# Kernel optimization log

Hardware: AMD Instinct MI355X
Metric: run time of the kernel (lower is better)

Reference implementation:

```python
import jax, jax.numpy as jnp
import numpy as np

NUM_HEADS = 16


def setup_inputs() -> dict:
    rng = jax.random.key(0)
    ks = jax.random.split(rng, 11)
    T, B, E = 1024, 4, 1024
    s = E ** -0.5  # weight init scale
    return {
        "query": jax.random.normal(ks[0], (T, B, E), jnp.float32),
        "key": jax.random.normal(ks[1], (T, B, E), jnp.float32),
        "value": jax.random.normal(ks[2], (T, B, E), jnp.float32),
        "q_proj_weight": jax.random.normal(ks[3], (E, E), jnp.float32) * s,
        "k_proj_weight1": jax.random.normal(ks[4], (E, E), jnp.float32) * s,
        "k_proj_weight2": jax.random.normal(ks[5], (E, E), jnp.float32) * s,
        "v_proj_weight": jax.random.normal(ks[6], (E, E), jnp.float32) * s,
        "in_proj_bias": jax.random.normal(ks[7], (4 * E,), jnp.float32) * 0.02,
        "out_proj_weight": jax.random.normal(ks[8], (E, E), jnp.float32) * s,
        "out_proj_bias": jax.random.normal(ks[9], (E,), jnp.float32) * 0.02,
        "pi": jax.random.uniform(ks[10], (2, NUM_HEADS), jnp.float32, 0.3, 0.7),
    }


def reference(query, key, value, q_proj_weight, k_proj_weight1, k_proj_weight2,
              v_proj_weight, in_proj_bias, out_proj_weight, out_proj_bias, pi):
    T, Bz, E = query.shape
    H = NUM_HEADS
    hd = E // H
    scaling = hd ** -0.5

    b_q, b_k1, b_k2, b_v = jnp.split(in_proj_bias, 4)
    q = query @ q_proj_weight.T + b_q
    k1 = key @ k_proj_weight1.T + b_k1
    k2 = key @ k_proj_weight2.T + b_k2
    v = value @ v_proj_weight.T + b_v

    def heads(x):  # (S, B, E) -> (B*H, S, hd)
        S = x.shape[0]
        return x.reshape(S, Bz * H, hd).transpose(1, 0, 2)

    q, k1, k2, v = heads(q), heads(k1), heads(k2), heads(v)

    def sqdist(a, b):  # (B*H, Nt, hd), (B*H, Ns, hd) -> (B*H, Nt, Ns)
        a2 = jnp.sum(a * a, axis=-1)
        b2 = jnp.sum(b * b, axis=-1)
        ab = jnp.einsum('btd,bsd->bts', a, b)
        return a2[:, :, None] + b2[:, None, :] - 2.0 * ab

    e1 = jnp.exp(-scaling / 2.0 * sqdist(q, k1))
    e2 = jnp.exp(-3.0 * scaling / 2.0 * sqdist(q, k2))

    pi1 = jnp.clip(jnp.abs(pi[0]), 1e-6, 2.0)  # (H,)
    pi2 = jnp.clip(jnp.abs(pi[1]), 1e-6, 2.0)

    Nt, Ns = e1.shape[1], e1.shape[2]
    attn = (e1.reshape(Bz, H, Nt, Ns) * pi1[None, :, None, None]
            + e2.reshape(Bz, H, Nt, Ns) * pi2[None, :, None, None])
    attn = attn.reshape(Bz * H, Nt, Ns)
    attn = attn / (jnp.sum(attn, axis=-1, keepdims=True) + 1e-6)

    out = jnp.einsum('bts,bsd->btd', attn, v)        # (B*H, Nt, hd)
    out = out.transpose(1, 0, 2).reshape(T, Bz, E)   # (T, B, E)
    return out @ out_proj_weight.T + out_proj_bias
```

## Files before the change

kernel.cpp:

```cpp
#include <hip/hip_runtime.h>
#include <hip/hip_bf16.h>

#define T_DIM 1024
#define B_DIM 4
#define E_DIM 1024
#define H_DIM 16
#define HD    64
#define M_DIM (T_DIM * B_DIM)

typedef __hip_bfloat16 bf16;
typedef __bf16 bf16x8 __attribute__((ext_vector_type(8)));
typedef __bf16 bf16x4 __attribute__((ext_vector_type(4)));
typedef float  f32x4  __attribute__((ext_vector_type(4)));

#define P4S ((size_t)M_DIM * E_DIM)
#define P1S ((size_t)E_DIM * E_DIM)

__global__ __launch_bounds__(256) void cvt_all(
    const float* __restrict__ q, const float* __restrict__ k,
    const float* __restrict__ v, const float* __restrict__ w0,
    const float* __restrict__ w1, const float* __restrict__ w2,
    const float* __restrict__ w3, const float* __restrict__ w4,
    __bf16* __restrict__ dst)
{
  size_t i = ((size_t)blockIdx.x * 256 + threadIdx.x) * 8;
  const float* src;
  size_t off;
  if (i < P4S)            { src = q; off = i; }
  else if (i < 2 * P4S)   { src = k; off = i - P4S; }
  else if (i < 3 * P4S)   { src = v; off = i - 2 * P4S; }
  else {
    size_t j = i - 3 * P4S;
    int wsel = (int)(j >> 20);
    off = j & (P1S - 1);
    const float* ws[5] = {w0, w1, w2, w3, w4};
    src = ws[wsel];
  }
  float4 a = *(const float4*)(src + off);
  float4 b = *(const float4*)(src + off + 4);
  bf16x8 o;
  o[0] = (__bf16)a.x; o[1] = (__bf16)a.y; o[2] = (__bf16)a.z; o[3] = (__bf16)a.w;
  o[4] = (__bf16)b.x; o[5] = (__bf16)b.y; o[6] = (__bf16)b.z; o[7] = (__bf16)b.w;
  *(bf16x8*)(dst + i) = o;
}

__device__ __forceinline__ void load_lds16(const __bf16* g, __bf16* l) {
  __builtin_amdgcn_global_load_lds(
      (__attribute__((address_space(1))) void*)(void*)g,
      (__attribute__((address_space(3))) void*)l, 16, 0, 0);
}

template <typename TO>
__device__ __forceinline__ void gemm_body(
    const __bf16* __restrict__ X, const __bf16* __restrict__ W,
    const float* __restrict__ bias, TO* __restrict__ C,
    int bm, int bn, int Ndim, int Kdim, __bf16* As, __bf16* Bs)
{
  const int tid  = threadIdx.x;
  const int lane = tid & 63;
  const int wave = tid >> 6;
  const int wy = (wave >> 1) * 64;
  const int wx = (wave & 1) * 64;
  const int mrow = lane & 15, quad = lane >> 4;

  const int srow = tid >> 2;
  const int ke   = (tid & 3) * 8;
  const __bf16* gA0 = X + (size_t)(bm + srow)      * Kdim + ke;
  const __bf16* gA1 = X + (size_t)(bm + srow + 64) * Kdim + ke;
  const __bf16* gB0 = W + (size_t)(bn + srow)      * Kdim + ke;
  const __bf16* gB1 = W + (size_t)(bn + srow + 64) * Kdim + ke;
  __bf16* lA0 = As + tid * 8;
  __bf16* lA1 = As + (tid + 256) * 8;
  __bf16* lB0 = Bs + tid * 8;
  __bf16* lB1 = Bs + (tid + 256) * 8;

  f32x4 acc[4][4];
#pragma unroll
  for (int i = 0; i < 4; ++i)
#pragma unroll
    for (int j = 0; j < 4; ++j) acc[i][j] = (f32x4)0.0f;

  for (int k0 = 0; k0 < Kdim; k0 += 32) {
    __syncthreads();
    load_lds16(gA0 + k0, lA0);
    load_lds16(gA1 + k0, lA1);
    load_lds16(gB0 + k0, lB0);
    load_lds16(gB1 + k0, lB1);
    __syncthreads();
    bf16x8 af[4], bf[4];
#pragma unroll
    for (int i = 0; i < 4; ++i)
      af[i] = *(const bf16x8*)(As + (wy + i * 16 + mrow) * 32 + quad * 8);
#pragma unroll
    for (int j = 0; j < 4; ++j)
      bf[j] = *(const bf16x8*)(Bs + (wx + j * 16 + mrow) * 32 + quad * 8);
#pragma unroll
    for (int i = 0; i < 4; ++i)
#pragma unroll
      for (int j = 0; j < 4; ++j)
        acc[i][j] = __builtin_amdgcn_mfma_f32_16x16x32_bf16(af[i], bf[j], acc[i][j], 0, 0, 0);
  }

#pragma unroll
  for (int j = 0; j < 4; ++j) {
    int col = bn + wx + j * 16 + mrow;
    float bc = bias[col];
#pragma unroll
    for (int i = 0; i < 4; ++i) {
      int rbase = bm + wy + i * 16 + quad * 4;
#pragma unroll
      for (int r = 0; r < 4; ++r)
        C[(size_t)(rbase + r) * Ndim + col] = (TO)(acc[i][j][r] + bc);
    }
  }
}

__global__ __launch_bounds__(256) void proj_gemm4(
    const __bf16* __restrict__ xbase, const __bf16* __restrict__ wbase,
    const float* __restrict__ bin, __bf16* __restrict__ cbase)
{
  __shared__ __bf16 As[128 * 32];
  __shared__ __bf16 Bs[128 * 32];
  const int z = blockIdx.z;
  const __bf16* X = xbase + ((z == 0) ? 0 : (z == 3) ? 2 * P4S : P4S);
  const __bf16* W = wbase + (size_t)z * P1S;
  const float* bias = bin + z * E_DIM;
  __bf16* C = cbase + (size_t)z * P4S;
  gemm_body<__bf16>(X, W, bias, C, blockIdx.x * 128, blockIdx.y * 128,
                    E_DIM, E_DIM, As, Bs);
}

__global__ __launch_bounds__(256) void out_gemm(
    const __bf16* __restrict__ X, const __bf16* __restrict__ W,
    const float* __restrict__ bias, float* __restrict__ C)
{
  __shared__ __bf16 As[128 * 32];
  __shared__ __bf16 Bs[128 * 32];
  gemm_body<float>(X, W, bias, C, blockIdx.x * 128, blockIdx.y * 128,
                   E_DIM, E_DIM, As, Bs);
}

__global__ __launch_bounds__(256) void head_norms(
    const __bf16* __restrict__ Qp, const __bf16* __restrict__ K1p,
    const __bf16* __restrict__ K2p, float* __restrict__ qn,
    float* __restrict__ kn1, float* __restrict__ kn2)
{
  int id = blockIdx.x * 256 + threadIdx.x;
  int which = id >> 16;
  int r = id & 65535;
  int bh = r >> 10, t = r & 1023;
  int b = bh >> 4, h = bh & 15;
  const __bf16* src = (which == 0) ? Qp : ((which == 1) ? K1p : K2p);
  float* dst = (which == 0) ? qn : ((which == 1) ? kn1 : kn2);
  const __bf16* p = src + (size_t)(t * 4 + b) * 1024 + h * 64;
  float s = 0.f;
#pragma unroll
  for (int c = 0; c < 8; ++c) {
    bf16x8 v = *(const bf16x8*)(p + c * 8);
#pragma unroll
    for (int j = 0; j < 8; ++j) { float x = (float)v[j]; s += x * x; }
  }
  dst[bh * 1024 + t] = s;
}

__global__ __launch_bounds__(256) void v_transpose(
    const __bf16* __restrict__ Vp, __bf16* __restrict__ Vt_g)
{
  const int bh = blockIdx.x, kt = blockIdx.y;
  const int b = bh >> 4, h = bh & 15;
  const int tid = threadIdx.x;
  __shared__ __bf16 tile[64][88];
  {
    int s = tid >> 2, d0 = (tid & 3) * 16;
    const __bf16* src = Vp + (size_t)((kt * 64 + s) * 4 + b) * 1024 + h * 64 + d0;
    *(bf16x8*)(&tile[s][d0])     = *(const bf16x8*)(src);
    *(bf16x8*)(&tile[s][d0 + 8]) = *(const bf16x8*)(src + 8);
  }
  __syncthreads();
#pragma unroll
  for (int c = 0; c < 2; ++c) {
    int idx = tid * 2 + c;
    int d = idx >> 3, u0 = (idx & 7) * 8;
    bf16x8 o;
#pragma unroll
    for (int i = 0; i < 8; ++i) {
      int u = u0 + i;
      int s = (u & 3) * 16 + (u >> 2);
      o[i] = tile[s][d];
    }
    *(bf16x8*)(Vt_g + ((size_t)bh * 64 + d) * 1024 + kt * 64 + u0) = o;
  }
}

__global__ __launch_bounds__(256, 2) void mgk_attn_mfma(
    const __bf16* __restrict__ Qp, const __bf16* __restrict__ K1p,
    const __bf16* __restrict__ K2p, const __bf16* __restrict__ Vt_g,
    const float* __restrict__ qn_g, const float* __restrict__ kn1_g,
    const float* __restrict__ kn2_g, const float* __restrict__ pi,
    __bf16* __restrict__ AO)
{
  __shared__ __bf16 lds[28672];
  __bf16* Qs  = lds;
  __bf16* K1s = lds + 8192;
  __bf16* K2s = lds + 12288;
  __bf16* Vt  = lds + 16384;
  __bf16* Pl  = lds + 20480;

  const int bh = blockIdx.x, qt = blockIdx.y;
  const int b = bh >> 4, h = bh & 15;
  const int tid = threadIdx.x, lane = tid & 63, w = tid >> 6;
  const int mrow = lane & 15, quad = lane >> 4;

  const float c1 = 0.0625f;
  const float c2 = 0.1875f;
  const float p1 = fminf(fmaxf(fabsf(pi[h]), 1e-6f), 2.0f);
  const float p2 = fminf(fmaxf(fabsf(pi[H_DIM + h]), 1e-6f), 2.0f);
  const int hoff = h * 64;

  f32x4 qnv[2];
#pragma unroll
  for (int i = 0; i < 2; ++i)
    qnv[i] = *(const f32x4*)(qn_g + bh * 1024 + qt * 128 + w * 32 + i * 16 + quad * 4);

#pragma unroll
  for (int wi = 0; wi < 4; ++wi) {
    int window = w * 4 + wi;
    int qr = window * 8 + (lane >> 3), c = lane & 7;
    const __bf16* src = Qp + (size_t)((qt * 128 + qr) * 4 + b) * 1024 + hoff
                        + ((c ^ (qr & 7)) << 3);
    load_lds16(src, Qs + window * 512 + lane * 8);
  }

  f32x4 oacc[2][4];
#pragma unroll
  for (int i = 0; i < 2; ++i)
#pragma unroll
    for (int j = 0; j < 4; ++j) oacc[i][j] = (f32x4)0.0f;
  f32x4 rsl[2] = {(f32x4)0.0f, (f32x4)0.0f};

  for (int kt = 0; kt < 16; ++kt) {
    __syncthreads();
#pragma unroll
    for (int wi = 0; wi < 2; ++wi) {
      int window = w * 2 + wi;
      int kr = window * 8 + (lane >> 3), c = lane & 7;
      size_t srow = (size_t)((kt * 64 + kr) * 4 + b) * 1024 + hoff;
      int off = (c ^ (kr & 7)) << 3;
      load_lds16(K1p + srow + off, K1s + window * 512 + lane * 8);
      load_lds16(K2p + srow + off, K2s + window * 512 + lane * 8);
      load_lds16(Vt_g + ((size_t)bh * 64 + kr) * 1024 + kt * 64 + off,
                 Vt + window * 512 + lane * 8);
    }
    float kn1j[4], kn2j[4];
#pragma unroll
    for (int j = 0; j < 4; ++j) {
      kn1j[j] = kn1_g[bh * 1024 + kt * 64 + j * 16 + mrow];
      kn2j[j] = kn2_g[bh * 1024 + kt * 64 + j * 16 + mrow];
    }
    __syncthreads();

    bf16x8 af[2][2];
#pragma unroll
    for (int i = 0; i < 2; ++i)
#pragma unroll
      for (int kk = 0; kk < 2; ++kk)
        af[i][kk] = *(const bf16x8*)(Qs + (w * 32 + i * 16 + mrow) * 64
                                     + (((kk * 4 + quad) ^ (mrow & 7)) << 3));
    f32x4 acc1[2][4], acc2[2][4];
#pragma unroll
    for (int i = 0; i < 2; ++i)
#pragma unroll
      for (int j = 0; j < 4; ++j) { acc1[i][j] = (f32x4)0.0f; acc2[i][j] = (f32x4)0.0f; }
#pragma unroll
    for (int kk = 0; kk < 2; ++kk)
#pragma unroll
      for (int j = 0; j < 4; ++j) {
        bf16x8 b1f = *(const bf16x8*)(K1s + (j * 16 + mrow) * 64
                                      + (((kk * 4 + quad) ^ (mrow & 7)) << 3));
        bf16x8 b2f = *(const bf16x8*)(K2s + (j * 16 + mrow) * 64
                                      + (((kk * 4 + quad) ^ (mrow & 7)) << 3));
#pragma unroll
        for (int i = 0; i < 2; ++i) {
          acc1[i][j] = __builtin_amdgcn_mfma_f32_16x16x32_bf16(af[i][kk], b1f, acc1[i][j], 0, 0, 0);
          acc2[i][j] = __builtin_amdgcn_mfma_f32_16x16x32_bf16(af[i][kk], b2f, acc2[i][j], 0, 0, 0);
        }
      }

#pragma unroll
    for (int i = 0; i < 2; ++i) {
      f32x4 pv[4];
#pragma unroll
      for (int j = 0; j < 4; ++j) {
        f32x4 p;
#pragma unroll
        for (int r = 0; r < 4; ++r) {
          float arg1 = c1 * (2.0f * acc1[i][j][r] - qnv[i][r] - kn1j[j]);
          float arg2 = c2 * (2.0f * acc2[i][j][r] - qnv[i][r] - kn2j[j]);
          p[r] = p1 * __expf(arg1) + p2 * __expf(arg2);
        }
        pv[j] = p;
        rsl[i] += p;
      }
#pragma unroll
      for (int r = 0; r < 4; ++r) {
        int q = i * 16 + quad * 4 + r;
        bf16x4 pk;
        pk[0] = (__bf16)pv[0][r]; pk[1] = (__bf16)pv[1][r];
        pk[2] = (__bf16)pv[2][r]; pk[3] = (__bf16)pv[3][r];
        int lc = mrow >> 1;
        *(bf16x4*)(Pl + w * 2048 + q * 64 + ((lc ^ (q & 7)) << 3) + (mrow & 1) * 4) = pk;
      }
    }
    __syncthreads();

    bf16x8 pf[2][2];
#pragma unroll
    for (int i = 0; i < 2; ++i)
#pragma unroll
      for (int kk = 0; kk < 2; ++kk)
        pf[i][kk] = *(const bf16x8*)(Pl + w * 2048 + (i * 16 + mrow) * 64
                                     + (((kk * 4 + quad) ^ (mrow & 7)) << 3));
#pragma unroll
    for (int kk = 0; kk < 2; ++kk)
#pragma unroll
      for (int j = 0; j < 4; ++j) {
        bf16x8 vf = *(const bf16x8*)(Vt + (j * 16 + mrow) * 64
                                     + (((kk * 4 + quad) ^ (mrow & 7)) << 3));
#pragma unroll
        for (int i = 0; i < 2; ++i)
          oacc[i][j] = __builtin_amdgcn_mfma_f32_16x16x32_bf16(pf[i][kk], vf, oacc[i][j], 0, 0, 0);
      }
  }

#pragma unroll
  for (int i = 0; i < 2; ++i)
#pragma unroll
    for (int d = 1; d < 16; d <<= 1) {
      f32x4 o;
#pragma unroll
      for (int r = 0; r < 4; ++r) o[r] = __shfl_xor(rsl[i][r], d, 64);
      rsl[i] += o;
    }

#pragma unroll
  for (int i = 0; i < 2; ++i) {
    f32x4 inv;
#pragma unroll
    for (int r = 0; r < 4; ++r) inv[r] = 1.0f / (rsl[i][r] + 1e-6f);
#pragma unroll
    for (int j = 0; j < 4; ++j) {
      int col = hoff + j * 16 + mrow;
#pragma unroll
      for (int r = 0; r < 4; ++r) {
        int t = qt * 128 + w * 32 + i * 16 + quad * 4 + r;
        AO[(size_t)(t * 4 + b) * 1024 + col] = (__bf16)(oacc[i][j][r] * inv[r]);
      }
    }
  }
}

extern "C" void kernel_launch(void* const* d_in, const int* in_sizes, int n_in,
                              void* d_out, int out_size, void* d_ws, size_t ws_size,
                              hipStream_t stream) {
  const float* query = (const float*)d_in[0];
  const float* key   = (const float*)d_in[1];
  const float* value = (const float*)d_in[2];
  const float* Wq    = (const float*)d_in[3];
  const float* Wk1   = (const float*)d_in[4];
  const float* Wk2   = (const float*)d_in[5];
  const float* Wv    = (const float*)d_in[6];
  const float* bin   = (const float*)d_in[7];
  const float* Wo    = (const float*)d_in[8];
  const float* bo    = (const float*)d_in[9];
  const float* pi    = (const float*)d_in[10];
  float* out = (float*)d_out;

  __bf16* qc  = (__bf16*)d_ws;
  __bf16* wq  = qc  + 3 * P4S;
  __bf16* wo  = wq  + 4 * P1S;
  __bf16* Qp  = wq  + 5 * P1S;
  __bf16* K1p = Qp  + P4S;
  __bf16* K2p = K1p + P4S;
  __bf16* Vp  = K2p + P4S;
  __bf16* AO  = Vp  + P4S;
  float*  qn_g  = (float*)(AO + P4S);
  float*  kn1_g = qn_g  + 64 * 1024;
  float*  kn2_g = kn1_g + 64 * 1024;
  __bf16* Vt_g  = qc;

  cvt_all<<<8704, 256, 0, stream>>>(query, key, value, Wq, Wk1, Wk2, Wv, Wo, qc);

  proj_gemm4<<<dim3(M_DIM / 128, E_DIM / 128, 4), 256, 0, stream>>>(qc, wq, bin, Qp);

  head_norms<<<768, 256, 0, stream>>>(Qp, K1p, K2p, qn_g, kn1_g, kn2_g);
  v_transpose<<<dim3(64, 16), 256, 0, stream>>>(Vp, Vt_g);

  mgk_attn_mfma<<<dim3(64, 8), 256, 0, stream>>>(
      Qp, K1p, K2p, Vt_g, qn_g, kn1_g, kn2_g, pi, AO);

  out_gemm<<<dim3(M_DIM / 128, E_DIM / 128), 256, 0, stream>>>(AO, wo, bo, out);
}
```

Before: 279.2 us.

## Pipeline attention K/V staging, fold constants into exp2, split-K output GEMM

Head-norm, V-transpose and output-bias initialization are merged into one prep kernel. The key norms are prescaled and log(pi) is folded into them, so the attention kernel uses raw exp2 with no multiplies by pi. The attention loop now prefetches the next K/V tile into LDS after reading fragments into registers, which removes one barrier per iteration. The output projection becomes a split-K=2 GEMM that accumulates into the bias-initialized output with float atomics. This trades a higher register count and atomic traffic for fewer launches and better overlap.

```diff
diff --git a/kernel.cpp b/kernel.cpp
--- a/kernel.cpp
+++ b/kernel.cpp
@@ -15,6 +15,9 @@
 
 #define P4S ((size_t)M_DIM * E_DIM)
 #define P1S ((size_t)E_DIM * E_DIM)
+
+#define C1F 0.0901684437f
+#define C2F 0.2705053270f
 
 __global__ __launch_bounds__(256) void cvt_all(
     const float* __restrict__ q, const float* __restrict__ k,
@@ -130,65 +133,135 @@
                     E_DIM, E_DIM, As, Bs);
 }
 
-__global__ __launch_bounds__(256) void out_gemm(
+__global__ __launch_bounds__(256) void out_gemm_sk(
     const __bf16* __restrict__ X, const __bf16* __restrict__ W,
-    const float* __restrict__ bias, float* __restrict__ C)
+    float* __restrict__ C)
 {
   __shared__ __bf16 As[128 * 32];
   __shared__ __bf16 Bs[128 * 32];
-  gemm_body<float>(X, W, bias, C, blockIdx.x * 128, blockIdx.y * 128,
-                   E_DIM, E_DIM, As, Bs);
-}
-
-__global__ __launch_bounds__(256) void head_norms(
+  const int tid  = threadIdx.x;
+  const int lane = tid & 63;
+  const int wave = tid >> 6;
+  const int wy = (wave >> 1) * 64;
+  const int wx = (wave & 1) * 64;
+  const int bm = blockIdx.x * 128, bn = blockIdx.y * 128;
+  const int kbeg = blockIdx.z * 512;
+  const int mrow = lane & 15, quad = lane >> 4;
+
+  const int srow = tid >> 2;
+  const int ke   = (tid & 3) * 8;
+  const __bf16* gA0 = X + (size_t)(bm + srow)      * E_DIM + kbeg + ke;
+  const __bf16* gA1 = X + (size_t)(bm + srow + 64) * E_DIM + kbeg + ke;
+  const __bf16* gB0 = W + (size_t)(bn + srow)      * E_DIM + kbeg + ke;
+  const __bf16* gB1 = W + (size_t)(bn + srow + 64) * E_DIM + kbeg + ke;
+  __bf16* lA0 = As + tid * 8;
+  __bf16* lA1 = As + (tid + 256) * 8;
+  __bf16* lB0 = Bs + tid * 8;
+  __bf16* lB1 = Bs + (tid + 256) * 8;
+
+  f32x4 acc[4][4];
+#pragma unroll
+  for (int i = 0; i < 4; ++i)
+#pragma unroll
+    for (int j = 0; j < 4; ++j) acc[i][j] = (f32x4)0.0f;
+
+  for (int k0 = 0; k0 < 512; k0 += 32) {
+    __syncthreads();
+    load_lds16(gA0 + k0, lA0);
+    load_lds16(gA1 + k0, lA1);
+    load_lds16(gB0 + k0, lB0);
+    load_lds16(gB1 + k0, lB1);
+    __syncthreads();
+    bf16x8 af[4], bf[4];
+#pragma unroll
+    for (int i = 0; i < 4; ++i)
+      af[i] = *(const bf16x8*)(As + (wy + i * 16 + mrow) * 32 + quad * 8);
+#pragma unroll
+    for (int j = 0; j < 4; ++j)
+      bf[j] = *(const bf16x8*)(Bs + (wx + j * 16 + mrow) * 32 + quad * 8);
+#pragma unroll
+    for (int i = 0; i < 4; ++i)
+#pragma unroll
+      for (int j = 0; j < 4; ++j)
+        acc[i][j] = __builtin_amdgcn_mfma_f32_16x16x32_bf16(af[i], bf[j], acc[i][j], 0, 0, 0);
+  }
+
+#pragma unroll
+  for (int j = 0; j < 4; ++j) {
+    int col = bn + wx + j * 16 + mrow;
+#pragma unroll
+    for (int i = 0; i < 4; ++i) {
+      int rbase = bm + wy + i * 16 + quad * 4;
+#pragma unroll
+      for (int r = 0; r < 4; ++r)
+        unsafeAtomicAdd(&C[(size_t)(rbase + r) * E_DIM + col], acc[i][j][r]);
+    }
+  }
+}
+
+__global__ __launch_bounds__(256) void prep(
     const __bf16* __restrict__ Qp, const __bf16* __restrict__ K1p,
-    const __bf16* __restrict__ K2p, float* __restrict__ qn,
-    float* __restrict__ kn1, float* __restrict__ kn2)
-{
-  int id = blockIdx.x * 256 + threadIdx.x;
-  int which = id >> 16;
-  int r = id & 65535;
-  int bh = r >> 10, t = r & 1023;
-  int b = bh >> 4, h = bh & 15;
-  const __bf16* src = (which == 0) ? Qp : ((which == 1) ? K1p : K2p);
-  float* dst = (which == 0) ? qn : ((which == 1) ? kn1 : kn2);
-  const __bf16* p = src + (size_t)(t * 4 + b) * 1024 + h * 64;
-  float s = 0.f;
-#pragma unroll
-  for (int c = 0; c < 8; ++c) {
-    bf16x8 v = *(const bf16x8*)(p + c * 8);
-#pragma unroll
-    for (int j = 0; j < 8; ++j) { float x = (float)v[j]; s += x * x; }
-  }
-  dst[bh * 1024 + t] = s;
-}
-
-__global__ __launch_bounds__(256) void v_transpose(
-    const __bf16* __restrict__ Vp, __bf16* __restrict__ Vt_g)
-{
-  const int bh = blockIdx.x, kt = blockIdx.y;
-  const int b = bh >> 4, h = bh & 15;
-  const int tid = threadIdx.x;
-  __shared__ __bf16 tile[64][88];
-  {
-    int s = tid >> 2, d0 = (tid & 3) * 16;
-    const __bf16* src = Vp + (size_t)((kt * 64 + s) * 4 + b) * 1024 + h * 64 + d0;
-    *(bf16x8*)(&tile[s][d0])     = *(const bf16x8*)(src);
-    *(bf16x8*)(&tile[s][d0 + 8]) = *(const bf16x8*)(src + 8);
-  }
-  __syncthreads();
-#pragma unroll
-  for (int c = 0; c < 2; ++c) {
-    int idx = tid * 2 + c;
-    int d = idx >> 3, u0 = (idx & 7) * 8;
-    bf16x8 o;
-#pragma unroll
-    for (int i = 0; i < 8; ++i) {
-      int u = u0 + i;
-      int s = (u & 3) * 16 + (u >> 2);
-      o[i] = tile[s][d];
-    }
-    *(bf16x8*)(Vt_g + ((size_t)bh * 64 + d) * 1024 + kt * 64 + u0) = o;
+    const __bf16* __restrict__ K2p, const __bf16* __restrict__ Vp,
+    const float* __restrict__ pi, const float* __restrict__ bo,
+    float* __restrict__ qn, float* __restrict__ kn1, float* __restrict__ kn2,
+    __bf16* __restrict__ Vt_g, float* __restrict__ out)
+{
+  const int bid = blockIdx.x, tid = threadIdx.x;
+  if (bid < 768) {
+    int id = bid * 256 + tid;
+    int which = id >> 16;
+    int r = id & 65535;
+    int bh = r >> 10, t = r & 1023;
+    int b = bh >> 4, h = bh & 15;
+    const __bf16* src = (which == 0) ? Qp : ((which == 1) ? K1p : K2p);
+    const __bf16* p = src + (size_t)(t * 4 + b) * 1024 + h * 64;
+    float s = 0.f;
+#pragma unroll
+    for (int c = 0; c < 8; ++c) {
+      bf16x8 v = *(const bf16x8*)(p + c * 8);
+#pragma unroll
+      for (int j = 0; j < 8; ++j) { float x = (float)v[j]; s += x * x; }
+    }
+    if (which == 0) {
+      qn[bh * 1024 + t] = s;
+    } else if (which == 1) {
+      float p1 = fminf(fmaxf(fabsf(pi[h]), 1e-6f), 2.0f);
+      kn1[bh * 1024 + t] = C1F * s - __builtin_amdgcn_logf(p1);
+    } else {
+      float p2 = fminf(fmaxf(fabsf(pi[H_DIM + h]), 1e-6f), 2.0f);
+      kn2[bh * 1024 + t] = C2F * s - __builtin_amdgcn_logf(p2);
+    }
+  } else if (bid < 1792) {
+    int idx = bid - 768;
+    int bh = idx >> 4, kt = idx & 15;
+    int b = bh >> 4, h = bh & 15;
+    __shared__ __bf16 tile[64][88];
+    {
+      int s = tid >> 2, d0 = (tid & 3) * 16;
+      const __bf16* src = Vp + (size_t)((kt * 64 + s) * 4 + b) * 1024 + h * 64 + d0;
+      *(bf16x8*)(&tile[s][d0])     = *(const bf16x8*)(src);
+      *(bf16x8*)(&tile[s][d0 + 8]) = *(const bf16x8*)(src + 8);
+    }
+    __syncthreads();
+#pragma unroll
+    for (int c = 0; c < 2; ++c) {
+      int idx2 = tid * 2 + c;
+      int d = idx2 >> 3, u0 = (idx2 & 7) * 8;
+      bf16x8 o;
+#pragma unroll
+      for (int i = 0; i < 8; ++i) {
+        int u = u0 + i;
+        int s = (u & 3) * 16 + (u >> 2);
+        o[i] = tile[s][d];
+      }
+      *(bf16x8*)(Vt_g + ((size_t)bh * 64 + d) * 1024 + kt * 64 + u0) = o;
+    }
+  } else {
+    int idx = (bid - 1792) * 256 + tid;
+    int base = idx * 16;
+#pragma unroll
+    for (int c = 0; c < 4; ++c)
+      *(float4*)(out + base + c * 4) = *(const float4*)(bo + ((base + c * 4) & 1023));
   }
 }
 
@@ -196,8 +269,7 @@
     const __bf16* __restrict__ Qp, const __bf16* __restrict__ K1p,
     const __bf16* __restrict__ K2p, const __bf16* __restrict__ Vt_g,
     const float* __restrict__ qn_g, const float* __restrict__ kn1_g,
-    const float* __restrict__ kn2_g, const float* __restrict__ pi,
-    __bf16* __restrict__ AO)
+    const float* __restrict__ kn2_g, __bf16* __restrict__ AO)
 {
   __shared__ __bf16 lds[28672];
   __bf16* Qs  = lds;
@@ -210,36 +282,19 @@
   const int b = bh >> 4, h = bh & 15;
   const int tid = threadIdx.x, lane = tid & 63, w = tid >> 6;
   const int mrow = lane & 15, quad = lane >> 4;
-
-  const float c1 = 0.0625f;
-  const float c2 = 0.1875f;
-  const float p1 = fminf(fmaxf(fabsf(pi[h]), 1e-6f), 2.0f);
-  const float p2 = fminf(fmaxf(fabsf(pi[H_DIM + h]), 1e-6f), 2.0f);
   const int hoff = h * 64;
 
-  f32x4 qnv[2];
-#pragma unroll
-  for (int i = 0; i < 2; ++i)
-    qnv[i] = *(const f32x4*)(qn_g + bh * 1024 + qt * 128 + w * 32 + i * 16 + quad * 4);
-
-#pragma unroll
-  for (int wi = 0; wi < 4; ++wi) {
-    int window = w * 4 + wi;
-    int qr = window * 8 + (lane >> 3), c = lane & 7;
-    const __bf16* src = Qp + (size_t)((qt * 128 + qr) * 4 + b) * 1024 + hoff
-                        + ((c ^ (qr & 7)) << 3);
-    load_lds16(src, Qs + window * 512 + lane * 8);
-  }
-
-  f32x4 oacc[2][4];
-#pragma unroll
-  for (int i = 0; i < 2; ++i)
-#pragma unroll
-    for (int j = 0; j < 4; ++j) oacc[i][j] = (f32x4)0.0f;
-  f32x4 rsl[2] = {(f32x4)0.0f, (f32x4)0.0f};
-
-  for (int kt = 0; kt < 16; ++kt) {
-    __syncthreads();
+  const float TWO_C1 = 2.0f * C1F, TWO_C2 = 2.0f * C2F;
+
+  f32x4 s1v[2], s2v[2];
+#pragma unroll
+  for (int i = 0; i < 2; ++i) {
+    f32x4 q = *(const f32x4*)(qn_g + bh * 1024 + qt * 128 + w * 32 + i * 16 + quad * 4);
+    s1v[i] = C1F * q;
+    s2v[i] = C2F * q;
+  }
+
+  auto stageK = [&](int kt) {
 #pragma unroll
     for (int wi = 0; wi < 2; ++wi) {
       int window = w * 2 + wi;
@@ -251,53 +306,84 @@
       load_lds16(Vt_g + ((size_t)bh * 64 + kr) * 1024 + kt * 64 + off,
                  Vt + window * 512 + lane * 8);
     }
+  };
+
+#pragma unroll
+  for (int wi = 0; wi < 4; ++wi) {
+    int window = w * 4 + wi;
+    int qr = window * 8 + (lane >> 3), c = lane & 7;
+    const __bf16* src = Qp + (size_t)((qt * 128 + qr) * 4 + b) * 1024 + hoff
+                        + ((c ^ (qr & 7)) << 3);
+    load_lds16(src, Qs + window * 512 + lane * 8);
+  }
+  stageK(0);
+
+  f32x4 oacc[2][4];
+#pragma unroll
+  for (int i = 0; i < 2; ++i)
+#pragma unroll
+    for (int j = 0; j < 4; ++j) oacc[i][j] = (f32x4)0.0f;
+  f32x4 rsl[2] = {(f32x4)0.0f, (f32x4)0.0f};
+
+  __syncthreads();
+
+  bf16x8 af[2][2];
+#pragma unroll
+  for (int i = 0; i < 2; ++i)
+#pragma unroll
+    for (int kk = 0; kk < 2; ++kk)
+      af[i][kk] = *(const bf16x8*)(Qs + (w * 32 + i * 16 + mrow) * 64
+                                   + (((kk * 4 + quad) ^ (mrow & 7)) << 3));
+
+  for (int kt = 0; kt < 16; ++kt) {
     float kn1j[4], kn2j[4];
 #pragma unroll
     for (int j = 0; j < 4; ++j) {
       kn1j[j] = kn1_g[bh * 1024 + kt * 64 + j * 16 + mrow];
       kn2j[j] = kn2_g[bh * 1024 + kt * 64 + j * 16 + mrow];
     }
-    __syncthreads();
-
-    bf16x8 af[2][2];
+
+    bf16x8 b1f[2][4], b2f[2][4], vf[2][4];
+#pragma unroll
+    for (int kk = 0; kk < 2; ++kk)
+#pragma unroll
+      for (int j = 0; j < 4; ++j) {
+        int off = (j * 16 + mrow) * 64 + (((kk * 4 + quad) ^ (mrow & 7)) << 3);
+        b1f[kk][j] = *(const bf16x8*)(K1s + off);
+        b2f[kk][j] = *(const bf16x8*)(K2s + off);
+        vf[kk][j]  = *(const bf16x8*)(Vt  + off);
+      }
+    __syncthreads();
+
+    if (kt < 15) stageK(kt + 1);
+
+    f32x4 acc1[2][4], acc2[2][4];
 #pragma unroll
     for (int i = 0; i < 2; ++i)
 #pragma unroll
-      for (int kk = 0; kk < 2; ++kk)
-        af[i][kk] = *(const bf16x8*)(Qs + (w * 32 + i * 16 + mrow) * 64
-                                     + (((kk * 4 + quad) ^ (mrow & 7)) << 3));
-    f32x4 acc1[2][4], acc2[2][4];
-#pragma unroll
-    for (int i = 0; i < 2; ++i)
-#pragma unroll
       for (int j = 0; j < 4; ++j) { acc1[i][j] = (f32x4)0.0f; acc2[i][j] = (f32x4)0.0f; }
 #pragma unroll
     for (int kk = 0; kk < 2; ++kk)
 #pragma unroll
-      for (int j = 0; j < 4; ++j) {
-        bf16x8 b1f = *(const bf16x8*)(K1s + (j * 16 + mrow) * 64
-                                      + (((kk * 4 + quad) ^ (mrow & 7)) << 3));
-        bf16x8 b2f = *(const bf16x8*)(K2s + (j * 16 + mrow) * 64
-                                      + (((kk * 4 + quad) ^ (mrow & 7)) << 3));
+      for (int j = 0; j < 4; ++j)
 #pragma unroll
         for (int i = 0; i < 2; ++i) {
-          acc1[i][j] = __builtin_amdgcn_mfma_f32_16x16x32_bf16(af[i][kk], b1f, acc1[i][j], 0, 0, 0);
-          acc2[i][j] = __builtin_amdgcn_mfma_f32_16x16x32_bf16(af[i][kk], b2f, acc2[i][j], 0, 0, 0);
+          acc1[i][j] = __builtin_amdgcn_mfma_f32_16x16x32_bf16(af[i][kk], b1f[kk][j], acc1[i][j], 0, 0, 0);
+          acc2[i][j] = __builtin_amdgcn_mfma_f32_16x16x32_bf16(af[i][kk], b2f[kk][j], acc2[i][j], 0, 0, 0);
         }
-      }
 
 #pragma unroll
     for (int i = 0; i < 2; ++i) {
       f32x4 pv[4];
 #pragma unroll
       for (int j = 0; j < 4; ++j) {
+        f32x4 d1 = s1v[i] + kn1j[j];
+        f32x4 d2 = s2v[i] + kn2j[j];
         f32x4 p;
 #pragma unroll
-        for (int r = 0; r < 4; ++r) {
-          float arg1 = c1 * (2.0f * acc1[i][j][r] - qnv[i][r] - kn1j[j]);
-          float arg2 = c2 * (2.0f * acc2[i][j][r] - qnv[i][r] - kn2j[j]);
-          p[r] = p1 * __expf(arg1) + p2 * __expf(arg2);
-        }
+        for (int r = 0; r < 4; ++r)
+          p[r] = __builtin_amdgcn_exp2f(TWO_C1 * acc1[i][j][r] - d1[r])
+               + __builtin_amdgcn_exp2f(TWO_C2 * acc2[i][j][r] - d2[r]);
         pv[j] = p;
         rsl[i] += p;
       }
@@ -311,7 +397,6 @@
         *(bf16x4*)(Pl + w * 2048 + q * 64 + ((lc ^ (q & 7)) << 3) + (mrow & 1) * 4) = pk;
       }
     }
-    __syncthreads();
 
     bf16x8 pf[2][2];
 #pragma unroll
@@ -323,13 +408,12 @@
 #pragma unroll
     for (int kk = 0; kk < 2; ++kk)
 #pragma unroll
-      for (int j = 0; j < 4; ++j) {
-        bf16x8 vf = *(const bf16x8*)(Vt + (j * 16 + mrow) * 64
-                                     + (((kk * 4 + quad) ^ (mrow & 7)) << 3));
+      for (int j = 0; j < 4; ++j)
 #pragma unroll
         for (int i = 0; i < 2; ++i)
-          oacc[i][j] = __builtin_amdgcn_mfma_f32_16x16x32_bf16(pf[i][kk], vf, oacc[i][j], 0, 0, 0);
-      }
+          oacc[i][j] = __builtin_amdgcn_mfma_f32_16x16x32_bf16(pf[i][kk], vf[kk][j], oacc[i][j], 0, 0, 0);
+
+    if (kt < 15) __syncthreads();
   }
 
 #pragma unroll
@@ -392,11 +476,11 @@
 
   proj_gemm4<<<dim3(M_DIM / 128, E_DIM / 128, 4), 256, 0, stream>>>(qc, wq, bin, Qp);
 
-  head_norms<<<768, 256, 0, stream>>>(Qp, K1p, K2p, qn_g, kn1_g, kn2_g);
-  v_transpose<<<dim3(64, 16), 256, 0, stream>>>(Vp, Vt_g);
+  prep<<<2816, 256, 0, stream>>>(Qp, K1p, K2p, Vp, pi, bo,
+                                 qn_g, kn1_g, kn2_g, Vt_g, out);
 
   mgk_attn_mfma<<<dim3(64, 8), 256, 0, stream>>>(
-      Qp, K1p, K2p, Vt_g, qn_g, kn1_g, kn2_g, pi, AO);
-
-  out_gemm<<<dim3(M_DIM / 128, E_DIM / 128), 256, 0, stream>>>(AO, wo, bo, out);
-}
+      Qp, K1p, K2p, Vt_g, qn_g, kn1_g, kn2_g, AO);
+
+  out_gemm_sk<<<dim3(M_DIM / 128, E_DIM / 128, 2), 256, 0, stream>>>(AO, wo, out);
+}
```

New measurement: 290.8 us. +4.2%, slower.
